# Performance work log

Hardware: AMD Instinct MI355X
Metric: run time of the kernel (lower is better)

Reference implementation:

```python
import jax, jax.numpy as jnp
import numpy as np

# 2^22-point radix-2 DIT FFT; NOTE the original code applies tf.abs at EVERY
# recursion level (not just the top), so each butterfly stage is followed by a
# magnitude + recomplexification. We reproduce that exact (non-standard) math.
N = 1 << 22
STAGES = 22


def _bitrev_perm(n, bits):
    # vectorized bit-reversal permutation (the order induced by the even/odd
    # decimation inputs[0::2] / inputs[1::2] recursion)
    x = np.arange(n)
    r = np.zeros(n, dtype=np.int64)
    for b in range(bits):
        r = (r << 1) | ((x >> b) & 1)
    return r


_PERM = jnp.asarray(_bitrev_perm(N, STAGES))


def setup_inputs() -> dict:
    key = jax.random.key(0)
    x = jax.random.normal(key, (N,), dtype=jnp.float32)
    return {"x": x}


def reference(x):
    # base case of the recursion: length-1 leaves are the bit-reversed inputs
    y = x[_PERM].astype(jnp.complex64)
    for s in range(1, STAGES + 1):  # fixed log2(N) stages, not a data loop
        m = 1 << s                  # sub-FFT size at this stage
        yb = y.reshape(N // m, m)   # [num_blocks, m]
        e = yb[:, : m // 2]         # 'even' sub-results
        o = yb[:, m // 2:]          # 'odd'  sub-results
        # twiddles W(m, k) = exp(-2*pi*i*k/m)
        tw = jnp.exp(
            jnp.complex64(-2j * np.pi) * jnp.arange(m // 2, dtype=jnp.float32) / m
        ).astype(jnp.complex64)
        t = tw[None, :] * o
        # butterfly then tf.abs (applied at every level in the original)
        mag = jnp.abs(jnp.concatenate([e + t, e - t], axis=1)).reshape(N)
        y = mag.astype(jnp.complex64) if s < STAGES else mag
    return y  # float32 magnitudes, shape [N]
```

## Files before the change

### kernel.cpp

```cpp
#include <hip/hip_runtime.h>
#include <math.h>


#define NBITS 22
#define RSQ2 0.70710678118654752440f

__device__ __forceinline__ float hsqrt(float x) { return __builtin_amdgcn_sqrtf(x); }

__device__ __forceinline__ void bf(float& e, float& o, float c, float s) {
    float rp = fmaf(c, o, e);
    float rm = fmaf(-c, o, e);
    float im = s * o;
    float im2 = im * im;
    e = hsqrt(fmaf(rp, rp, im2));
    o = hsqrt(fmaf(rm, rm, im2));
}
__device__ __forceinline__ void bf0(float& e, float& o) {
    float a = e + o, b = e - o;
    e = fabsf(a); o = fabsf(b);
}
__device__ __forceinline__ void bfq(float& e, float& o) {
    float h = hsqrt(fmaf(e, e, o * o));
    e = h; o = h;
}

__device__ __constant__ float KC[16] = {
    1.f, 0.980785280f, 0.923879533f, 0.831469612f, 0.707106781f, 0.555570233f,
    0.382683432f, 0.195090322f, 0.f, -0.195090322f, -0.382683432f, -0.555570233f,
    -0.707106781f, -0.831469612f, -0.923879533f, -0.980785280f };
__device__ __constant__ float KS[16] = {
    0.f, 0.195090322f, 0.382683432f, 0.555570233f, 0.707106781f, 0.831469612f,
    0.923879533f, 0.980785280f, 1.f, 0.980785280f, 0.923879533f, 0.831469612f,
    0.707106781f, 0.555570233f, 0.382683432f, 0.195090322f };

template <int L>
__device__ __forceinline__ void radixN(float* v, float c, float s) {
    float ca[L], sa[L];
    ca[L - 1] = c; sa[L - 1] = s;
#pragma unroll
    for (int a = L - 1; a > 0; --a) {
        ca[a - 1] = fmaf(-2.f * sa[a], sa[a], 1.f);
        sa[a - 1] = 2.f * sa[a] * ca[a];
    }
#pragma unroll
    for (int a = 0; a < L; ++a) {
        const int half = 1 << a;
#pragma unroll
        for (int d = 0; d < half; ++d) {
            const int k = d << (4 - a);
            float cd = fmaf(ca[a], KC[k], -sa[a] * KS[k]);
            float sd = fmaf(sa[a], KC[k],  ca[a] * KS[k]);
#pragma unroll
            for (int g = d; g < (1 << L); g += 2 * half)
                bf(v[g], v[g + half], cd, sd);
        }
    }
}

__device__ __forceinline__ void radix8z(float v[8]) {
    bf0(v[0], v[1]); bf0(v[2], v[3]); bf0(v[4], v[5]); bf0(v[6], v[7]);
    bf0(v[0], v[2]); bf0(v[4], v[6]);
    bfq(v[1], v[3]); bfq(v[5], v[7]);
    bf0(v[0], v[4]);
    bf(v[1], v[5], RSQ2, RSQ2);
    bfq(v[2], v[6]);
    bf(v[3], v[7], -RSQ2, RSQ2);
}

__global__ __launch_bounds__(256, 8) void fft_perm(const float* __restrict__ x,
                                                   float* __restrict__ y) {
    __shared__ float lds[64 * 65];
    const unsigned tid = threadIdx.x;
    const unsigned tx = tid & 63, g = tid >> 6;
    const unsigned C0 = (blockIdx.x & 31) * 64;
    const unsigned B0 = (blockIdx.x >> 5) * 64;

#pragma unroll
    for (int k = 0; k < 16; ++k) {
        unsigned r = g * 16 + k;
        unsigned a = __brev(C0 + r) >> (32 - 11);
        lds[r * 65 + tx] = x[a * 2048u + B0 + tx];
    }
    __syncthreads();

    float v[8];
#pragma unroll
    for (int q = 0; q < 2; ++q) {
        unsigned task = tid + 256u * q;
        unsigned c = task >> 3, grp = task & 7;
#pragma unroll
        for (int j = 0; j < 8; ++j) v[j] = lds[(grp * 8 + j) * 65 + c];
        radix8z(v);
        unsigned pr = __brev(B0 + c) >> (32 - 11);
        float* dst = y + pr * 2048u + C0 + grp * 8;
        *(float4*)(dst)     = make_float4(v[0], v[1], v[2], v[3]);
        *(float4*)(dst + 4) = make_float4(v[4], v[5], v[6], v[7]);
    }
}

__global__ __launch_bounds__(256, 4) void fft_low(float* __restrict__ y) {
    __shared__ float lds[8448];
    const unsigned t = threadIdx.x;
    const unsigned base = blockIdx.x * 8192;
    const unsigned lo = t & 7, hi = t >> 3;
    float v[32];

    {
        const float* src = y + base + lo + 256u * hi;
#pragma unroll
        for (int j = 0; j < 32; ++j) v[j] = src[8 * j];
        float r = (float)lo * (1.f / 256.f);
        radixN<5>(v, __builtin_amdgcn_cosf(r), __builtin_amdgcn_sinf(r));
#pragma unroll
        for (int j = 0; j < 32; ++j) {
            unsigned q = lo + 8u * j + 256u * hi;
            lds[q + (q >> 5)] = v[j];
        }
    }
    __syncthreads();

    {
#pragma unroll
        for (int j = 0; j < 32; ++j) {
            unsigned q = t + 256u * j;
            v[j] = lds[q + (q >> 5)];
        }
        float r = (float)t * (1.f / 8192.f);
        radixN<5>(v, __builtin_amdgcn_cosf(r), __builtin_amdgcn_sinf(r));
        float* dst = y + base + t;
#pragma unroll
        for (int j = 0; j < 32; ++j) dst[256u * j] = v[j];
    }
}

__global__ __launch_bounds__(256, 4) void fft_high(float* __restrict__ y) {
    __shared__ float lds[512 * 17 + 32];
    const unsigned tt = threadIdx.x;
    const unsigned li = tt & 15, u5 = tt >> 4;
    const unsigned low = blockIdx.x * 16 + li;
    float v[32];

    {
        const float* src = y + low;
#pragma unroll
        for (int j = 0; j < 32; ++j) v[j] = src[8192u * (32u * u5 + j)];
        float r = (float)low * (1.f / 262144.f);
        radixN<5>(v, __builtin_amdgcn_cosf(r), __builtin_amdgcn_sinf(r));
#pragma unroll
        for (int j = 0; j < 32; ++j) {
            unsigned trow = 32u * u5 + j;
            lds[trow * 17 + (trow >> 5) + li] = v[j];
        }
    }
    __syncthreads();

#pragma unroll
    for (int b = 0; b < 2; ++b) {
        const unsigned t0 = 2u * u5 + b;
        float* w = v + 16 * b;
#pragma unroll
        for (int j = 0; j < 16; ++j) {
            unsigned trow = t0 + 32u * j;
            w[j] = lds[trow * 17 + (trow >> 5) + li];
        }
        float r = ((float)low + 8192.f * (float)t0) * (1.f / 4194304.f);
        radixN<4>(w, __builtin_amdgcn_cosf(r), __builtin_amdgcn_sinf(r));
#pragma unroll
        for (int j = 0; j < 16; ++j)
            y[low + 8192u * (t0 + 32u * j)] = w[j];
    }
}

extern "C" void kernel_launch(void* const* d_in, const int* in_sizes, int n_in,
                              void* d_out, int out_size, void* d_ws, size_t ws_size,
                              hipStream_t stream) {
    const float* x = (const float*)d_in[0];
    float* out = (float*)d_out;

    fft_perm<<<dim3(1024), dim3(256), 0, stream>>>(x, out);
    fft_low<<<dim3(512), dim3(256), 0, stream>>>(out);
    fft_high<<<dim3(512), dim3(256), 0, stream>>>(out);
}
```

Baseline: 100.6 us.

## Fuse three FFT kernels into one cooperative kernel with grid syncs

Merges the permutation, low-stage, and high-stage kernels into a single cooperative kernel of 512 blocks, with grid.sync between phases in place of separate launches. The permutation phase now processes two tiles per block. The twiddle tables become constexpr so the compiler can fold them as immediates instead of reading constant memory. This removes two kernel launch gaps, at the cost of grid-wide barrier overhead and occupancy limited to 2 blocks per CU by the launch bounds.

```diff
diff --git a/kernel.cpp b/kernel.cpp
--- a/kernel.cpp
+++ b/kernel.cpp
@@ -1,8 +1,10 @@
 #include <hip/hip_runtime.h>
+#include <hip/hip_cooperative_groups.h>
 #include <math.h>
 
+namespace cg = cooperative_groups;
 
-#define NBITS 22
+
 #define RSQ2 0.70710678118654752440f
 
 __device__ __forceinline__ float hsqrt(float x) { return __builtin_amdgcn_sqrtf(x); }
@@ -24,11 +26,11 @@
     e = h; o = h;
 }
 
-__device__ __constant__ float KC[16] = {
+constexpr float KCc[16] = {
     1.f, 0.980785280f, 0.923879533f, 0.831469612f, 0.707106781f, 0.555570233f,
     0.382683432f, 0.195090322f, 0.f, -0.195090322f, -0.382683432f, -0.555570233f,
     -0.707106781f, -0.831469612f, -0.923879533f, -0.980785280f };
-__device__ __constant__ float KS[16] = {
+constexpr float KSc[16] = {
     0.f, 0.195090322f, 0.382683432f, 0.555570233f, 0.707106781f, 0.831469612f,
     0.923879533f, 0.980785280f, 1.f, 0.980785280f, 0.923879533f, 0.831469612f,
     0.707106781f, 0.555570233f, 0.382683432f, 0.195090322f };
@@ -48,8 +50,8 @@
 #pragma unroll
         for (int d = 0; d < half; ++d) {
             const int k = d << (4 - a);
-            float cd = fmaf(ca[a], KC[k], -sa[a] * KS[k]);
-            float sd = fmaf(sa[a], KC[k],  ca[a] * KS[k]);
+            float cd = fmaf(ca[a], KCc[k], -sa[a] * KSc[k]);
+            float sd = fmaf(sa[a], KCc[k],  ca[a] * KSc[k]);
 #pragma unroll
             for (int g = d; g < (1 << L); g += 2 * half)
                 bf(v[g], v[g + half], cd, sd);
@@ -67,107 +69,113 @@
     bf(v[3], v[7], -RSQ2, RSQ2);
 }
 
-__global__ __launch_bounds__(256, 8) void fft_perm(const float* __restrict__ x,
-                                                   float* __restrict__ y) {
-    __shared__ float lds[64 * 65];
+__global__ __launch_bounds__(256, 2) void fft_fused(const float* __restrict__ x,
+                                                    float* __restrict__ y) {
+    __shared__ float lds[8752];
+    cg::grid_group grid = cg::this_grid();
     const unsigned tid = threadIdx.x;
-    const unsigned tx = tid & 63, g = tid >> 6;
-    const unsigned C0 = (blockIdx.x & 31) * 64;
-    const unsigned B0 = (blockIdx.x >> 5) * 64;
+    const unsigned bid = blockIdx.x;
+
+    {
+        const unsigned tx = tid & 63, g = tid >> 6;
+#pragma unroll
+        for (int q = 0; q < 2; ++q) {
+            const unsigned tile = bid * 2u + q;
+            const unsigned C0 = (tile & 31) * 64;
+            const unsigned B0 = (tile >> 5) * 64;
+#pragma unroll
+            for (int k = 0; k < 16; ++k) {
+                unsigned r = g * 16 + k;
+                unsigned a = __brev(C0 + r) >> (32 - 11);
+                lds[r * 65 + tx] = x[a * 2048u + B0 + tx];
+            }
+            __syncthreads();
+            float v[8];
+#pragma unroll
+            for (int qq = 0; qq < 2; ++qq) {
+                unsigned task = tid + 256u * qq;
+                unsigned c = task >> 3, grp = task & 7;
+#pragma unroll
+                for (int j = 0; j < 8; ++j) v[j] = lds[(grp * 8 + j) * 65 + c];
+                radix8z(v);
+                unsigned pr = __brev(B0 + c) >> (32 - 11);
+                float* dst = y + pr * 2048u + C0 + grp * 8;
+                *(float4*)(dst)     = make_float4(v[0], v[1], v[2], v[3]);
+                *(float4*)(dst + 4) = make_float4(v[4], v[5], v[6], v[7]);
+            }
+            __syncthreads();
+        }
+    }
+    grid.sync();
+
+    {
+        const unsigned base = bid * 8192u;
+        const unsigned lo = tid & 7, hi = tid >> 3;
+        float v[32];
+
+        {
+            const float* src = y + base + lo + 256u * hi;
+#pragma unroll
+            for (int j = 0; j < 32; ++j) v[j] = src[8 * j];
+            float r = (float)lo * (1.f / 256.f);
+            radixN<5>(v, __builtin_amdgcn_cosf(r), __builtin_amdgcn_sinf(r));
+#pragma unroll
+            for (int j = 0; j < 32; ++j) {
+                unsigned q = lo + 8u * j + 256u * hi;
+                lds[q + (q >> 5)] = v[j];
+            }
+        }
+        __syncthreads();
+
+        {
+#pragma unroll
+            for (int j = 0; j < 32; ++j) {
+                unsigned q = tid + 256u * j;
+                v[j] = lds[q + (q >> 5)];
+            }
+            float r = (float)tid * (1.f / 8192.f);
+            radixN<5>(v, __builtin_amdgcn_cosf(r), __builtin_amdgcn_sinf(r));
+            float* dst = y + base + tid;
+#pragma unroll
+            for (int j = 0; j < 32; ++j) dst[256u * j] = v[j];
+        }
+    }
+    grid.sync();
+
+    {
+        const unsigned li = tid & 15, u5 = tid >> 4;
+        const unsigned low = bid * 16u + li;
+        float v[32];
+
+        {
+            const float* src = y + low;
+#pragma unroll
+            for (int j = 0; j < 32; ++j) v[j] = src[8192u * (32u * u5 + j)];
+            float r = (float)low * (1.f / 262144.f);
+            radixN<5>(v, __builtin_amdgcn_cosf(r), __builtin_amdgcn_sinf(r));
+#pragma unroll
+            for (int j = 0; j < 32; ++j) {
+                unsigned trow = 32u * u5 + j;
+                lds[trow * 17 + (trow >> 5) + li] = v[j];
+            }
+        }
+        __syncthreads();
 
 #pragma unroll
-    for (int k = 0; k < 16; ++k) {
-        unsigned r = g * 16 + k;
-        unsigned a = __brev(C0 + r) >> (32 - 11);
-        lds[r * 65 + tx] = x[a * 2048u + B0 + tx];
-    }
-    __syncthreads();
-
-    float v[8];
+        for (int b = 0; b < 2; ++b) {
+            const unsigned t0 = 2u * u5 + b;
+            float* w = v + 16 * b;
 #pragma unroll
-    for (int q = 0; q < 2; ++q) {
-        unsigned task = tid + 256u * q;
-        unsigned c = task >> 3, grp = task & 7;
+            for (int j = 0; j < 16; ++j) {
+                unsigned trow = t0 + 32u * j;
+                w[j] = lds[trow * 17 + (trow >> 5) + li];
+            }
+            float r = ((float)low + 8192.f * (float)t0) * (1.f / 4194304.f);
+            radixN<4>(w, __builtin_amdgcn_cosf(r), __builtin_amdgcn_sinf(r));
 #pragma unroll
-        for (int j = 0; j < 8; ++j) v[j] = lds[(grp * 8 + j) * 65 + c];
-        radix8z(v);
-        unsigned pr = __brev(B0 + c) >> (32 - 11);
-        float* dst = y + pr * 2048u + C0 + grp * 8;
-        *(float4*)(dst)     = make_float4(v[0], v[1], v[2], v[3]);
-        *(float4*)(dst + 4) = make_float4(v[4], v[5], v[6], v[7]);
-    }
-}
-
-__global__ __launch_bounds__(256, 4) void fft_low(float* __restrict__ y) {
-    __shared__ float lds[8448];
-    const unsigned t = threadIdx.x;
-    const unsigned base = blockIdx.x * 8192;
-    const unsigned lo = t & 7, hi = t >> 3;
-    float v[32];
-
-    {
-        const float* src = y + base + lo + 256u * hi;
-#pragma unroll
-        for (int j = 0; j < 32; ++j) v[j] = src[8 * j];
-        float r = (float)lo * (1.f / 256.f);
-        radixN<5>(v, __builtin_amdgcn_cosf(r), __builtin_amdgcn_sinf(r));
-#pragma unroll
-        for (int j = 0; j < 32; ++j) {
-            unsigned q = lo + 8u * j + 256u * hi;
-            lds[q + (q >> 5)] = v[j];
+            for (int j = 0; j < 16; ++j)
+                y[low + 8192u * (t0 + 32u * j)] = w[j];
         }
-    }
-    __syncthreads();
-
-    {
-#pragma unroll
-        for (int j = 0; j < 32; ++j) {
-            unsigned q = t + 256u * j;
-            v[j] = lds[q + (q >> 5)];
-        }
-        float r = (float)t * (1.f / 8192.f);
-        radixN<5>(v, __builtin_amdgcn_cosf(r), __builtin_amdgcn_sinf(r));
-        float* dst = y + base + t;
-#pragma unroll
-        for (int j = 0; j < 32; ++j) dst[256u * j] = v[j];
-    }
-}
-
-__global__ __launch_bounds__(256, 4) void fft_high(float* __restrict__ y) {
-    __shared__ float lds[512 * 17 + 32];
-    const unsigned tt = threadIdx.x;
-    const unsigned li = tt & 15, u5 = tt >> 4;
-    const unsigned low = blockIdx.x * 16 + li;
-    float v[32];
-
-    {
-        const float* src = y + low;
-#pragma unroll
-        for (int j = 0; j < 32; ++j) v[j] = src[8192u * (32u * u5 + j)];
-        float r = (float)low * (1.f / 262144.f);
-        radixN<5>(v, __builtin_amdgcn_cosf(r), __builtin_amdgcn_sinf(r));
-#pragma unroll
-        for (int j = 0; j < 32; ++j) {
-            unsigned trow = 32u * u5 + j;
-            lds[trow * 17 + (trow >> 5) + li] = v[j];
-        }
-    }
-    __syncthreads();
-
-#pragma unroll
-    for (int b = 0; b < 2; ++b) {
-        const unsigned t0 = 2u * u5 + b;
-        float* w = v + 16 * b;
-#pragma unroll
-        for (int j = 0; j < 16; ++j) {
-            unsigned trow = t0 + 32u * j;
-            w[j] = lds[trow * 17 + (trow >> 5) + li];
-        }
-        float r = ((float)low + 8192.f * (float)t0) * (1.f / 4194304.f);
-        radixN<4>(w, __builtin_amdgcn_cosf(r), __builtin_amdgcn_sinf(r));
-#pragma unroll
-        for (int j = 0; j < 16; ++j)
-            y[low + 8192u * (t0 + 32u * j)] = w[j];
     }
 }
 
@@ -177,7 +185,7 @@
     const float* x = (const float*)d_in[0];
     float* out = (float*)d_out;
 
-    fft_perm<<<dim3(1024), dim3(256), 0, stream>>>(x, out);
-    fft_low<<<dim3(512), dim3(256), 0, stream>>>(out);
-    fft_high<<<dim3(512), dim3(256), 0, stream>>>(out);
+    void* args[] = { (void*)&x, (void*)&out };
+    hipLaunchCooperativeKernel((const void*)fft_fused, dim3(512), dim3(256),
+                               args, 0, stream);
 }
```

New measurement: 235.3 us. 134% more time.
